# Performance work log

Measured on AMD Instinct MI355X. Metric: run time of the kernel, lower is better.

Reference implementation:

```python
import jax, jax.numpy as jnp
import numpy as np

S, B, D_IN, D_OUT, E, R = 2048, 8, 1024, 4096, 8, 16

def setup_inputs() -> dict:
    key = jax.random.key(0)
    ks = jax.random.split(key, 6)
    x = jax.random.normal(ks[0], (S, B, D_IN), dtype=jnp.float32)
    gate_w = jax.random.normal(ks[1], (E, D_IN), dtype=jnp.float32) * 0.01  # std=0.01 init
    gate_b = jnp.zeros((E,), dtype=jnp.float32)  # init_lambda = 0
    W = jax.random.normal(ks[2], (D_OUT, D_IN), dtype=jnp.float32) * 0.02
    bias = jax.random.normal(ks[3], (D_OUT,), dtype=jnp.float32) * 0.02
    lora_A = jax.random.normal(ks[4], (E, R, D_IN), dtype=jnp.float32) * 0.02
    lora_B = jax.random.normal(ks[5], (E, D_OUT, R), dtype=jnp.float32) * 0.02
    return {"x": x, "gate_w": gate_w, "gate_b": gate_b, "W": W, "bias": bias,
            "lora_A": lora_A, "lora_B": lora_B}

def reference(x, gate_w, gate_b, W, bias, lora_A, lora_B):
    # gate: Linear(hidden, E) applied tokenwise, then mean over seq dim (dim 0, batch_first=False)
    gates = jnp.einsum('sbd,ed->sbe', x, gate_w) + gate_b      # [S,B,E]
    gate_weights = gates.mean(axis=0)                           # [B,E]
    # per-expert LoRA delta (detached in the torch original)
    delta = jnp.einsum('eor,eri->eoi', lora_B, lora_A)          # [E,D_OUT,D_IN]
    delta = jax.lax.stop_gradient(delta)
    # per-sample merged weight: W + sum_e g[b,e] * delta[e]
    W_b = W[None] + jnp.einsum('be,eoi->boi', gate_weights, delta)  # [B,D_OUT,D_IN]
    # per-sample linear (equivalent to looping functional_call over samples)
    out = jnp.einsum('sbi,boi->sbo', x, W_b) + bias             # [S,B,D_OUT]
    return out
```

## Files before the change

### kernel.cpp

```cpp
#include <hip/hip_runtime.h>
#include <stdint.h>

typedef unsigned short u16;
typedef __bf16 bf16x8 __attribute__((ext_vector_type(8)));
typedef float  f32x4  __attribute__((ext_vector_type(4)));

#define SDIM 2048
#define BDIM 8
#define DIN  1024
#define DOUT 4096
#define EDIM 8
#define RDIM 16
#define KAUG 1152
#define MDIM (SDIM*BDIM)
#define SCH  32
#define NT2  18

__device__ __forceinline__ u16 f2bf(float f) {
    __bf16 h = (__bf16)f;
    return __builtin_bit_cast(u16, h);
}

__device__ __forceinline__ void gload16(const u16* g, u16* lds) {
    __builtin_amdgcn_global_load_lds(
        (const __attribute__((address_space(1))) void*)g,
        (__attribute__((address_space(3))) void*)lds, 16, 0, 0);
}

#define VMCNT(n)  asm volatile("s_waitcnt vmcnt(" #n ")" ::: "memory")
#define LGKM0()   asm volatile("s_waitcnt lgkmcnt(0)" ::: "memory")
#define BARF()    do { asm volatile("" ::: "memory");                \
                       __builtin_amdgcn_s_barrier();                 \
                       asm volatile("" ::: "memory"); } while (0)

__global__ __launch_bounds__(256) void k1_reduce_convert(
    const float* __restrict__ x, u16* __restrict__ Xb, float* __restrict__ P)
{
    const int b  = blockIdx.x;
    const int sc = blockIdx.y;
    const int i  = threadIdx.x * 4;
    float a0 = 0.f, a1 = 0.f, a2 = 0.f, a3 = 0.f;
    const int s0 = sc * (SDIM / SCH);
    for (int s = s0; s < s0 + (SDIM / SCH); ++s) {
        const float4 v = *reinterpret_cast<const float4*>(
            &x[((size_t)s * BDIM + b) * DIN + i]);
        a0 += v.x; a1 += v.y; a2 += v.z; a3 += v.w;
        ushort4 u{f2bf(v.x), f2bf(v.y), f2bf(v.z), f2bf(v.w)};
        *reinterpret_cast<ushort4*>(&Xb[((size_t)s * BDIM + b) * KAUG + i]) = u;
    }
    float4 p{a0, a1, a2, a3};
    *reinterpret_cast<float4*>(&P[((size_t)sc * BDIM + b) * DIN + i]) = p;
}

__global__ __launch_bounds__(256) void k2_gates(
    const float* __restrict__ P, const float* __restrict__ gw,
    const float* __restrict__ gb, float* __restrict__ g)
{
    const int e = blockIdx.x, b = blockIdx.y, t = threadIdx.x;
    float dot = 0.f;
    for (int i = t; i < DIN; i += 256) {
        float xs = 0.f;
        #pragma unroll
        for (int c = 0; c < SCH; ++c) xs += P[((size_t)c * BDIM + b) * DIN + i];
        dot += xs * gw[(size_t)e * DIN + i];
    }
    __shared__ float red[256];
    red[t] = dot;
    __syncthreads();
    #pragma unroll
    for (int off = 128; off > 0; off >>= 1) {
        if (t < off) red[t] += red[t + off];
        __syncthreads();
    }
    if (t == 0) g[b * EDIM + e] = red[0] * (1.0f / SDIM) + gb[e];
}

__global__ __launch_bounds__(256) void kw_build_waug(
    const float* __restrict__ W, const float* __restrict__ lb, u16* __restrict__ Waug)
{
    const int o = blockIdx.x, t = threadIdx.x;
    for (int i = t; i < DIN; i += 256)
        Waug[(size_t)o * KAUG + i] = f2bf(W[(size_t)o * DIN + i]);
    if (t < EDIM * RDIM) {
        const int e = t >> 4, r = t & 15;
        Waug[(size_t)o * KAUG + DIN + t] =
            f2bf(lb[((size_t)e * DOUT + o) * RDIM + r]);
    }
}

__global__ __launch_bounds__(256) void kl_convert(
    const float* __restrict__ la, u16* __restrict__ LAb)
{
    const int idx = blockIdx.x * 256 + threadIdx.x;
    if (idx < EDIM * RDIM * DIN) LAb[idx] = f2bf(la[idx]);
}

__global__ __launch_bounds__(256) void k4_scale_u(
    const float* __restrict__ T, const float* __restrict__ g, u16* __restrict__ Xb)
{
    const int idx = blockIdx.x * 256 + threadIdx.x;
    const int m = idx >> 7, er = idx & 127;
    const int b = m & (BDIM - 1), e = er >> 4;
    const float u = g[b * EDIM + e] * T[idx];
    Xb[(size_t)m * KAUG + DIN + er] = f2bf(u);
}

template <int ADD_BIAS>
__global__ __launch_bounds__(256) void gemm_bt(
    const u16* __restrict__ A, int lda,
    const u16* __restrict__ B, int ldb,
    float* __restrict__ C, int ldc,
    const float* __restrict__ bias, int ktiles)
{
    __shared__ __align__(16) u16 As[128][64];
    __shared__ __align__(16) u16 Bs[128][64];

    const int tid  = threadIdx.x;
    const int lane = tid & 63;
    const int l15  = lane & 15;
    const int l4   = lane >> 4;
    const int sw   = lane & 7;
    const int wid  = tid >> 6;
    const int wr   = wid >> 1;
    const int wc   = wid & 1;
    const int m0 = blockIdx.y * 128;
    const int n0 = blockIdx.x * 128;

    f32x4 acc[4][4] = {};

    for (int kt = 0; kt < ktiles; ++kt) {
        #pragma unroll
        for (int ii = 0; ii < 4; ++ii) {
            const int cix = ii * 256 + tid;
            const int row = cix >> 3, cl = cix & 7;
            const int kof = kt * 64 + ((cl ^ (row & 7)) << 3);
            gload16(A + (size_t)(m0 + row) * lda + kof, &As[0][0] + cix * 8);
            gload16(B + (size_t)(n0 + row) * ldb + kof, &Bs[0][0] + cix * 8);
        }
        __syncthreads();
        #pragma unroll
        for (int ks = 0; ks < 2; ++ks) {
            bf16x8 av[4], bv[4];
            #pragma unroll
            for (int mi = 0; mi < 4; ++mi)
                av[mi] = *reinterpret_cast<const bf16x8*>(
                    &As[wr * 64 + mi * 16 + l15][((ks * 4 + l4) ^ sw) << 3]);
            #pragma unroll
            for (int ni = 0; ni < 4; ++ni)
                bv[ni] = *reinterpret_cast<const bf16x8*>(
                    &Bs[wc * 64 + ni * 16 + l15][((ks * 4 + l4) ^ sw) << 3]);
            #pragma unroll
            for (int mi = 0; mi < 4; ++mi)
                #pragma unroll
                for (int ni = 0; ni < 4; ++ni)
                    acc[mi][ni] = __builtin_amdgcn_mfma_f32_16x16x32_bf16(
                        av[mi], bv[ni], acc[mi][ni], 0, 0, 0);
        }
        __syncthreads();
    }

    #pragma unroll
    for (int mi = 0; mi < 4; ++mi) {
        const int r0 = m0 + wr * 64 + mi * 16 + l4 * 4;
        #pragma unroll
        for (int ni = 0; ni < 4; ++ni) {
            const int col = n0 + wc * 64 + ni * 16 + l15;
            const float badd = ADD_BIAS ? bias[col] : 0.0f;
            float* cp = C + (size_t)r0 * ldc + col;
            #pragma unroll
            for (int r = 0; r < 4; ++r)
                cp[(size_t)r * ldc] = acc[mi][ni][r] + badd;
        }
    }
}

__global__ __launch_bounds__(512) void gemm_main(
    const u16* __restrict__ A, const u16* __restrict__ Bm,
    float* __restrict__ C, const float* __restrict__ bias)
{
    __shared__ __align__(16) u16 As[2][2][128][64];
    __shared__ __align__(16) u16 Bs[2][2][128][64];

    const int tid  = threadIdx.x;
    const int lane = tid & 63;
    const int l15  = lane & 15;
    const int l4   = lane >> 4;
    const int sw   = lane & 7;
    const int wid  = tid >> 6;
    const int wm   = wid >> 2;
    const int wn   = wid & 3;
    const int bh   = wn >> 1;
    const int bl   = wn & 1;

    const int f   = blockIdx.x + blockIdx.y * gridDim.x;
    const int cpx = (gridDim.x * gridDim.y) >> 3;
    const int s_  = (f & 7) * cpx + (f >> 3);
    const int m0  = (s_ / gridDim.x) * 256;
    const int n0  = (s_ % gridDim.x) * 256;

    f32x4  acc[8][4] = {};
    bf16x8 aq[2][2], bv[4][2];

    auto stage = [&](int s) {
        const int t = s >> 2, part = s & 3, buf = t & 1, hf = part & 1;
        #pragma unroll
        for (int ii = 0; ii < 2; ++ii) {
            const int cix = ii * 512 + tid;
            const int row = cix >> 3, cl = cix & 7;
            const int kof = t * 64 + ((cl ^ (row & 7)) << 3);
            if (part < 2)
                gload16(A + (size_t)(m0 + hf * 128 + row) * KAUG + kof,
                        &As[buf][hf][0][0] + cix * 8);
            else
                gload16(Bm + (size_t)(n0 + hf * 128 + row) * KAUG + kof,
                        &Bs[buf][hf][0][0] + cix * 8);
        }
    };

    #define STG(SU) do { const int su_ = (SU); if (su_ < 4 * NT2) stage(su_); } while (0)
    #define RD_BV(BUF)                                                        \
        _Pragma("unroll") for (int nf = 0; nf < 4; ++nf)                      \
            _Pragma("unroll") for (int kk = 0; kk < 2; ++kk)                  \
                bv[nf][kk] = *reinterpret_cast<const bf16x8*>(                \
                    &Bs[BUF][bh][bl * 64 + nf * 16 + l15]                     \
                       [((kk * 4 + l4) ^ sw) << 3]);
    #define RD_AQ(BUF, Q)                                                     \
        _Pragma("unroll") for (int fr = 0; fr < 2; ++fr)                      \
            _Pragma("unroll") for (int kk = 0; kk < 2; ++kk)                  \
                aq[fr][kk] = *reinterpret_cast<const bf16x8*>(                \
                    &As[BUF][wm][(Q) * 32 + fr * 16 + l15]                    \
                       [((kk * 4 + l4) ^ sw) << 3]);
    #define MMA(Q)                                                            \
        do {                                                                  \
            __builtin_amdgcn_s_setprio(1);                                    \
            _Pragma("unroll") for (int kk = 0; kk < 2; ++kk)                  \
                _Pragma("unroll") for (int fr = 0; fr < 2; ++fr)              \
                    _Pragma("unroll") for (int nf = 0; nf < 4; ++nf)          \
                        acc[(Q) * 2 + fr][nf] =                               \
                            __builtin_amdgcn_mfma_f32_16x16x32_bf16(          \
                                aq[fr][kk], bv[nf][kk],                       \
                                acc[(Q) * 2 + fr][nf], 0, 0, 0);              \
            __builtin_amdgcn_s_setprio(0);                                    \
        } while (0)

    stage(0); stage(1); stage(2); stage(3); stage(4);
    VMCNT(2);
    BARF();

    for (int j = 0; j < NT2; ++j) {
        const int buf = j & 1;
        RD_BV(buf);
        RD_AQ(buf, 0);
        STG(4 * j + 5);
        BARF();
        LGKM0();
        __builtin_amdgcn_sched_barrier(0);
        MMA(0);
        BARF();
        RD_AQ(buf, 1);
        STG(4 * j + 6);
        BARF();
        LGKM0();
        __builtin_amdgcn_sched_barrier(0);
        MMA(1);
        BARF();
        RD_AQ(buf, 2);
        STG(4 * j + 7);
        BARF();
        LGKM0();
        __builtin_amdgcn_sched_barrier(0);
        MMA(2);
        BARF();
        RD_AQ(buf, 3);
        STG(4 * j + 8);
        if (j < NT2 - 2) { VMCNT(2); } else { VMCNT(0); }
        BARF();
        LGKM0();
        __builtin_amdgcn_sched_barrier(0);
        MMA(3);
        BARF();
    }
    #undef STG
    #undef RD_BV
    #undef RD_AQ
    #undef MMA

    #pragma unroll
    for (int a = 0; a < 8; ++a) {
        const int row0 = m0 + wm * 128 + a * 16 + l4 * 4;
        #pragma unroll
        for (int nf = 0; nf < 4; ++nf) {
            const int col = n0 + wn * 64 + nf * 16 + l15;
            const float badd = bias[col];
            float* cp = C + (size_t)row0 * DOUT + col;
            #pragma unroll
            for (int q = 0; q < 4; ++q)
                cp[(size_t)q * DOUT] = acc[a][nf][q] + badd;
        }
    }
}

extern "C" void kernel_launch(void* const* d_in, const int* in_sizes, int n_in,
                              void* d_out, int out_size, void* d_ws, size_t ws_size,
                              hipStream_t stream)
{
    const float* x    = (const float*)d_in[0];
    const float* gw   = (const float*)d_in[1];
    const float* gb   = (const float*)d_in[2];
    const float* W    = (const float*)d_in[3];
    const float* bias = (const float*)d_in[4];
    const float* la   = (const float*)d_in[5];
    const float* lb   = (const float*)d_in[6];
    float* out = (float*)d_out;

    char* ws = (char*)d_ws;
    u16*   Xb   = (u16*)(ws);
    u16*   Waug = (u16*)(ws + 37748736);
    float* T    = (float*)(ws + 47185920);
    float* P    = (float*)(ws + 55574528);
    u16*   LAb  = (u16*)(ws + 56623104);
    float* G    = (float*)(ws + 56885248);

    k1_reduce_convert<<<dim3(BDIM, SCH), 256, 0, stream>>>(x, Xb, P);
    kw_build_waug<<<DOUT, 256, 0, stream>>>(W, lb, Waug);
    kl_convert<<<(EDIM * RDIM * DIN + 255) / 256, 256, 0, stream>>>(la, LAb);
    k2_gates<<<dim3(EDIM, BDIM), 256, 0, stream>>>(P, gw, gb, G);
    gemm_bt<0><<<dim3(1, MDIM / 128), 256, 0, stream>>>(
        Xb, KAUG, LAb, DIN, T, EDIM * RDIM, nullptr, DIN / 64);
    k4_scale_u<<<(MDIM * EDIM * RDIM) / 256, 256, 0, stream>>>(T, G, Xb);
    gemm_main<<<dim3(DOUT / 256, MDIM / 256), 512, 0, stream>>>(
        Xb, Waug, out, bias);
}
```

Measured before the change: 243.9 us.

## Fuse gate scaling into LoRA GEMM epilogue and reorder main GEMM staging

```diff
diff --git a/kernel.cpp b/kernel.cpp
--- a/kernel.cpp
+++ b/kernel.cpp
@@ -95,22 +95,9 @@
     if (idx < EDIM * RDIM * DIN) LAb[idx] = f2bf(la[idx]);
 }
 
-__global__ __launch_bounds__(256) void k4_scale_u(
-    const float* __restrict__ T, const float* __restrict__ g, u16* __restrict__ Xb)
-{
-    const int idx = blockIdx.x * 256 + threadIdx.x;
-    const int m = idx >> 7, er = idx & 127;
-    const int b = m & (BDIM - 1), e = er >> 4;
-    const float u = g[b * EDIM + e] * T[idx];
-    Xb[(size_t)m * KAUG + DIN + er] = f2bf(u);
-}
-
-template <int ADD_BIAS>
-__global__ __launch_bounds__(256) void gemm_bt(
-    const u16* __restrict__ A, int lda,
-    const u16* __restrict__ B, int ldb,
-    float* __restrict__ C, int ldc,
-    const float* __restrict__ bias, int ktiles)
+__global__ __launch_bounds__(256) void gemm_lora(
+    const u16* __restrict__ A, const u16* __restrict__ B,
+    const float* __restrict__ G, u16* __restrict__ Xb)
 {
     __shared__ __align__(16) u16 As[128][64];
     __shared__ __align__(16) u16 Bs[128][64];
@@ -124,18 +111,17 @@
     const int wr   = wid >> 1;
     const int wc   = wid & 1;
     const int m0 = blockIdx.y * 128;
-    const int n0 = blockIdx.x * 128;
 
     f32x4 acc[4][4] = {};
 
-    for (int kt = 0; kt < ktiles; ++kt) {
+    for (int kt = 0; kt < DIN / 64; ++kt) {
         #pragma unroll
         for (int ii = 0; ii < 4; ++ii) {
             const int cix = ii * 256 + tid;
             const int row = cix >> 3, cl = cix & 7;
             const int kof = kt * 64 + ((cl ^ (row & 7)) << 3);
-            gload16(A + (size_t)(m0 + row) * lda + kof, &As[0][0] + cix * 8);
-            gload16(B + (size_t)(n0 + row) * ldb + kof, &Bs[0][0] + cix * 8);
+            gload16(A + (size_t)(m0 + row) * KAUG + kof, &As[0][0] + cix * 8);
+            gload16(B + (size_t)row * DIN + kof, &Bs[0][0] + cix * 8);
         }
         __syncthreads();
         #pragma unroll
@@ -164,12 +150,14 @@
         const int r0 = m0 + wr * 64 + mi * 16 + l4 * 4;
         #pragma unroll
         for (int ni = 0; ni < 4; ++ni) {
-            const int col = n0 + wc * 64 + ni * 16 + l15;
-            const float badd = ADD_BIAS ? bias[col] : 0.0f;
-            float* cp = C + (size_t)r0 * ldc + col;
-            #pragma unroll
-            for (int r = 0; r < 4; ++r)
-                cp[(size_t)r * ldc] = acc[mi][ni][r] + badd;
+            const int col = wc * 64 + ni * 16 + l15;
+            const int e   = col >> 4;
+            #pragma unroll
+            for (int r = 0; r < 4; ++r) {
+                const int row = r0 + r;
+                const float gv = G[((row & 7) << 3) + e];
+                Xb[(size_t)row * KAUG + DIN + col] = f2bf(gv * acc[mi][ni][r]);
+            }
         }
     }
 }
@@ -193,31 +181,37 @@
     const int bl   = wn & 1;
 
     const int f   = blockIdx.x + blockIdx.y * gridDim.x;
-    const int cpx = (gridDim.x * gridDim.y) >> 3;
-    const int s_  = (f & 7) * cpx + (f >> 3);
-    const int m0  = (s_ / gridDim.x) * 256;
-    const int n0  = (s_ % gridDim.x) * 256;
+    const int xcd = f & 7, k = f >> 3;
+    const int gn  = xcd & 3, gm = xcd >> 2;
+    const int n0  = (gn * 4 + (k & 3)) * 256;
+    const int m0  = (gm * 32 + (k >> 2)) * 256;
 
     f32x4  acc[8][4] = {};
     bf16x8 aq[2][2], bv[4][2];
 
-    auto stage = [&](int s) {
-        const int t = s >> 2, part = s & 3, buf = t & 1, hf = part & 1;
+    auto stageA = [&](int t, int hf) {
+        const int buf = t & 1;
         #pragma unroll
         for (int ii = 0; ii < 2; ++ii) {
             const int cix = ii * 512 + tid;
             const int row = cix >> 3, cl = cix & 7;
             const int kof = t * 64 + ((cl ^ (row & 7)) << 3);
-            if (part < 2)
-                gload16(A + (size_t)(m0 + hf * 128 + row) * KAUG + kof,
-                        &As[buf][hf][0][0] + cix * 8);
-            else
-                gload16(Bm + (size_t)(n0 + hf * 128 + row) * KAUG + kof,
-                        &Bs[buf][hf][0][0] + cix * 8);
+            gload16(A + (size_t)(m0 + hf * 128 + row) * KAUG + kof,
+                    &As[buf][hf][0][0] + cix * 8);
         }
     };
-
-    #define STG(SU) do { const int su_ = (SU); if (su_ < 4 * NT2) stage(su_); } while (0)
+    auto stageB = [&](int t, int hf) {
+        const int buf = t & 1;
+        #pragma unroll
+        for (int ii = 0; ii < 2; ++ii) {
+            const int cix = ii * 512 + tid;
+            const int row = cix >> 3, cl = cix & 7;
+            const int kof = t * 64 + ((cl ^ (row & 7)) << 3);
+            gload16(Bm + (size_t)(n0 + hf * 128 + row) * KAUG + kof,
+                    &Bs[buf][hf][0][0] + cix * 8);
+        }
+    };
+
     #define RD_BV(BUF)                                                        \
         _Pragma("unroll") for (int nf = 0; nf < 4; ++nf)                      \
             _Pragma("unroll") for (int kk = 0; kk < 2; ++kk)                  \
@@ -243,44 +237,44 @@
             __builtin_amdgcn_s_setprio(0);                                    \
         } while (0)
 
-    stage(0); stage(1); stage(2); stage(3); stage(4);
-    VMCNT(2);
+    stageA(0, 0); stageA(0, 1); stageB(0, 0); stageB(0, 1);
+    stageA(1, 0); stageA(1, 1); stageB(1, 0); stageB(1, 1);
+    VMCNT(8);
     BARF();
 
     for (int j = 0; j < NT2; ++j) {
         const int buf = j & 1;
         RD_BV(buf);
         RD_AQ(buf, 0);
-        STG(4 * j + 5);
+        if (j >= 1 && j + 1 < NT2) stageA(j + 1, 0);
         BARF();
         LGKM0();
         __builtin_amdgcn_sched_barrier(0);
         MMA(0);
         BARF();
         RD_AQ(buf, 1);
-        STG(4 * j + 6);
+        if (j >= 1 && j + 1 < NT2) stageA(j + 1, 1);
         BARF();
         LGKM0();
         __builtin_amdgcn_sched_barrier(0);
         MMA(1);
         BARF();
         RD_AQ(buf, 2);
-        STG(4 * j + 7);
+        if (j + 2 < NT2) stageB(j + 2, 0);
         BARF();
         LGKM0();
         __builtin_amdgcn_sched_barrier(0);
         MMA(2);
         BARF();
         RD_AQ(buf, 3);
-        STG(4 * j + 8);
-        if (j < NT2 - 2) { VMCNT(2); } else { VMCNT(0); }
+        if (j + 2 < NT2) stageB(j + 2, 1);
         BARF();
         LGKM0();
         __builtin_amdgcn_sched_barrier(0);
         MMA(3);
-        BARF();
-    }
-    #undef STG
+        if (j <= NT2 - 3) { VMCNT(4); } else { VMCNT(0); }
+        BARF();
+    }
     #undef RD_BV
     #undef RD_AQ
     #undef MMA
@@ -316,18 +310,15 @@
     char* ws = (char*)d_ws;
     u16*   Xb   = (u16*)(ws);
     u16*   Waug = (u16*)(ws + 37748736);
-    float* T    = (float*)(ws + 47185920);
-    float* P    = (float*)(ws + 55574528);
-    u16*   LAb  = (u16*)(ws + 56623104);
-    float* G    = (float*)(ws + 56885248);
+    float* P    = (float*)(ws + 47185920);
+    u16*   LAb  = (u16*)(ws + 48234496);
+    float* G    = (float*)(ws + 48496640);
 
     k1_reduce_convert<<<dim3(BDIM, SCH), 256, 0, stream>>>(x, Xb, P);
     kw_build_waug<<<DOUT, 256, 0, stream>>>(W, lb, Waug);
     kl_convert<<<(EDIM * RDIM * DIN + 255) / 256, 256, 0, stream>>>(la, LAb);
     k2_gates<<<dim3(EDIM, BDIM), 256, 0, stream>>>(P, gw, gb, G);
-    gemm_bt<0><<<dim3(1, MDIM / 128), 256, 0, stream>>>(
-        Xb, KAUG, LAb, DIN, T, EDIM * RDIM, nullptr, DIN / 64);
-    k4_scale_u<<<(MDIM * EDIM * RDIM) / 256, 256, 0, stream>>>(T, G, Xb);
+    gemm_lora<<<dim3(1, MDIM / 128), 256, 0, stream>>>(Xb, LAb, G, Xb);
     gemm_main<<<dim3(DOUT / 256, MDIM / 256), 512, 0, stream>>>(
         Xb, Waug, out, bias);
 }
```

Result: slower. 249.0 us (+2.1%).
